# Kernel tuning notes

Hardware: AMD Instinct MI355X
Metric: run time of the kernel (lower is better)

## Reference

```python
import jax, jax.numpy as jnp
import numpy as np

N_NODES = 50000
N_EDGES = 800000
IN_CH = 128
HID_CH = 128
OUT_CH = 10
NUM_GRAPHS = 128


def setup_inputs() -> dict:
    key = jax.random.key(0)
    ks = jax.random.split(key, 10)
    x = jax.random.normal(ks[0], (N_NODES, IN_CH), dtype=jnp.float32)
    edge_index = jax.random.randint(ks[1], (2, N_EDGES), 0, N_NODES, dtype=jnp.int64)
    batch = jnp.sort(jax.random.randint(ks[2], (N_NODES,), 0, NUM_GRAPHS, dtype=jnp.int64))
    s1 = 1.0 / np.sqrt(IN_CH)
    s2 = 1.0 / np.sqrt(HID_CH)
    W1 = jax.random.uniform(ks[3], (IN_CH, HID_CH), jnp.float32, -s1, s1)
    b1 = jnp.zeros((HID_CH,), jnp.float32)
    W2 = jax.random.uniform(ks[4], (HID_CH, HID_CH), jnp.float32, -s2, s2)
    b2 = jnp.zeros((HID_CH,), jnp.float32)
    Wc = jax.random.uniform(ks[5], (HID_CH, OUT_CH), jnp.float32, -s2, s2)
    bc = jax.random.uniform(ks[6], (OUT_CH,), jnp.float32, -s2, s2)
    return {"x": x, "edge_index": edge_index, "batch": batch,
            "W1": W1, "b1": b1, "W2": W2, "b2": b2, "Wc": Wc, "bc": bc}


def _gcn_norm(edge_index, num_nodes):
    # add self-loops, compute symmetric normalization deg^-1/2[src]*deg^-1/2[dst]
    loop = jnp.arange(num_nodes, dtype=edge_index.dtype)
    src = jnp.concatenate([edge_index[0], loop])
    dst = jnp.concatenate([edge_index[1], loop])
    deg = jax.ops.segment_sum(jnp.ones_like(dst, dtype=jnp.float32), dst,
                              num_segments=num_nodes)
    dinv = jnp.where(deg > 0, jax.lax.rsqrt(deg), 0.0)
    norm = dinv[src] * dinv[dst]
    return src, dst, norm


def _gcn_conv(h, src, dst, norm, W, b, num_nodes):
    h = h @ W                                    # [N, out]
    msg = h[src] * norm[:, None]                 # [E+N, out] gather + scale
    agg = jax.ops.segment_sum(msg, dst, num_segments=num_nodes)
    return agg + b


def reference(x, edge_index, batch, W1, b1, W2, b2, Wc, bc):
    n = x.shape[0]
    src, dst, norm = _gcn_norm(edge_index, n)
    h = jax.nn.relu(_gcn_conv(x, src, dst, norm, W1, b1, n))
    h = jax.nn.relu(_gcn_conv(h, src, dst, norm, W2, b2, n))
    # global mean pool over graphs
    sums = jax.ops.segment_sum(h, batch, num_segments=NUM_GRAPHS)
    cnts = jax.ops.segment_sum(jnp.ones((n,), jnp.float32), batch,
                               num_segments=NUM_GRAPHS)
    pooled = sums / jnp.maximum(cnts, 1.0)[:, None]
    # dropout is identity in eval mode
    return pooled @ Wc + bc
```

## Files before the change

### kernel.cpp

```cpp
#include <hip/hip_runtime.h>

#define N_NODES 50000
#define N_EDGES 800000
#define CH 128
#define NOUT 10
#define NUM_GRAPHS 128
#define GR 64
#define GEMM_BLOCKS ((N_NODES + GR - 1) / GR)
#define FILL_SEGS 200
#define FILL_CHUNK (N_EDGES / FILL_SEGS)
#define FILL_BLOCKS (FILL_SEGS * 8)
#define DST_RANGE (N_NODES / 8)
#define DEG_CAP 64

typedef __attribute__((ext_vector_type(8))) short bf16x8;
typedef __attribute__((ext_vector_type(4))) float f32x4;

union FragU { uint4 u; bf16x8 s; };

__device__ __forceinline__ unsigned pack_bf16(float a, float b) {
    unsigned ua = __float_as_uint(a), ub = __float_as_uint(b);
    ua += 0x7fffu + ((ua >> 16) & 1u);
    ub += 0x7fffu + ((ub >> 16) & 1u);
    return (ua >> 16) | (ub & 0xffff0000u);
}

__device__ __forceinline__ unsigned short cvt_bf16(float v) {
    unsigned u = __float_as_uint(v);
    u += 0x7fffu + ((u >> 16) & 1u);
    return (unsigned short)(u >> 16);
}

__global__ __launch_bounds__(256) void k_prep(const float* __restrict__ W1,
                                              const float* __restrict__ W2,
                                              unsigned short* __restrict__ Wb1,
                                              unsigned short* __restrict__ Wb2,
                                              int* __restrict__ fill_pos,
                                              float* __restrict__ psum) {
    if (blockIdx.x < 2) {
        const float* W = blockIdx.x ? W2 : W1;
        unsigned short* Wb = blockIdx.x ? Wb2 : Wb1;
        for (int i = threadIdx.x; i < CH * CH; i += 256) {
            int k = i >> 7, n = i & 127;
            Wb[((((k >> 3) << 7) + n) << 3) + (k & 7)] = cvt_bf16(W[i]);
        }
    } else if (blockIdx.x < 198) {
        int idx = (blockIdx.x - 2) * 256 + threadIdx.x;
        if (idx < N_NODES) fill_pos[idx] = 0;
    } else {
        psum[(blockIdx.x - 198) * 256 + threadIdx.x] = 0.f;
    }
}

template <bool SCALE, bool ABF16>
__device__ __forceinline__ void gemm_body9(const void* __restrict__ X,
                                           const unsigned short* __restrict__ Wb,
                                           unsigned short* __restrict__ Yb,
                                           const int* __restrict__ cnt,
                                           int bid) {
    const int tid = threadIdx.x;
    const int w = tid >> 6;
    const int lane = tid & 63;
    const int m = lane & 15;
    const int quad = lane >> 4;
    const int row0 = bid * GR + w * 16;

    int row_a = row0 + m;
    if (row_a > N_NODES - 1) row_a = N_NODES - 1;

    FragU af[4];
    if (ABF16) {
        const uint4* Xr = (const uint4*)((const unsigned short*)X + (size_t)row_a * CH);
        #pragma unroll
        for (int ks = 0; ks < 4; ++ks) af[ks].u = Xr[ks * 4 + quad];
    } else {
        const float4* Xr = (const float4*)((const float*)X + (size_t)row_a * CH) + quad * 2;
        float4 a[8];
        #pragma unroll
        for (int ks = 0; ks < 4; ++ks) {
            a[ks * 2]     = Xr[ks * 8];
            a[ks * 2 + 1] = Xr[ks * 8 + 1];
        }
        #pragma unroll
        for (int ks = 0; ks < 4; ++ks) {
            af[ks].u.x = pack_bf16(a[ks * 2].x, a[ks * 2].y);
            af[ks].u.y = pack_bf16(a[ks * 2].z, a[ks * 2].w);
            af[ks].u.z = pack_bf16(a[ks * 2 + 1].x, a[ks * 2 + 1].y);
            af[ks].u.w = pack_bf16(a[ks * 2 + 1].z, a[ks * 2 + 1].w);
        }
    }

    f32x4 acc[8];
    #pragma unroll
    for (int ct = 0; ct < 8; ++ct) acc[ct] = (f32x4){0.f, 0.f, 0.f, 0.f};

    const uint4* Wq = (const uint4*)Wb;
    #pragma unroll
    for (int ks = 0; ks < 4; ++ks) {
        const int kg = ks * 4 + quad;
        #pragma unroll
        for (int ct = 0; ct < 8; ++ct) {
            FragU bfu;
            bfu.u = Wq[kg * 128 + m * 8 + ct];
            acc[ct] = __builtin_amdgcn_mfma_f32_16x16x32_bf16(af[ks].s, bfu.s, acc[ct], 0, 0, 0);
        }
    }

    #pragma unroll
    for (int r = 0; r < 4; ++r) {
        int row = row0 + quad * 4 + r;
        if (row < N_NODES) {
            float s = SCALE ? rsqrtf((float)(cnt[row] + 1)) : 1.0f;
            uint4 o;
            o.x = pack_bf16(acc[0][r] * s, acc[1][r] * s);
            o.y = pack_bf16(acc[2][r] * s, acc[3][r] * s);
            o.z = pack_bf16(acc[4][r] * s, acc[5][r] * s);
            o.w = pack_bf16(acc[6][r] * s, acc[7][r] * s);
            *(uint4*)(Yb + (size_t)row * CH + m * 8) = o;
        }
    }
}

__global__ __launch_bounds__(256) void k_gemm_fill(const float* __restrict__ X,
                                                   const unsigned short* __restrict__ Wb,
                                                   unsigned short* __restrict__ Yb,
                                                   const int* __restrict__ src,
                                                   const int* __restrict__ dst,
                                                   int* __restrict__ fill_pos,
                                                   int* __restrict__ csr_src) {
    if (blockIdx.x < FILL_BLOCKS) {
        const int b = blockIdx.x;
        const int rng = b & 7;
        const int seg = b >> 3;
        const int lo = rng * DST_RANGE, hi = lo + DST_RANGE;
        const int base = seg * FILL_CHUNK;
        for (int it = threadIdx.x * 4; it < FILL_CHUNK; it += 1024) {
            int e = base + it;
            int4 d4 = *(const int4*)(dst + e);
            int4 s4 = *(const int4*)(src + e);
            #pragma unroll
            for (int k = 0; k < 4; ++k) {
                int d = (&d4.x)[k];
                if (d >= lo && d < hi) {
                    int slot = atomicAdd(&fill_pos[d], 1);
                    if (slot < DEG_CAP) csr_src[(d << 6) + slot] = (&s4.x)[k];
                }
            }
        }
    } else {
        gemm_body9<false, false>(X, Wb, Yb, nullptr, blockIdx.x - FILL_BLOCKS);
    }
}

__global__ __launch_bounds__(256) void k_gemm9b(const unsigned short* __restrict__ Xb,
                                                const unsigned short* __restrict__ Wb,
                                                unsigned short* __restrict__ Yb,
                                                const int* __restrict__ cnt) {
    gemm_body9<true, true>(Xb, Wb, Yb, cnt, blockIdx.x);
}

__device__ __forceinline__ void acc_row(float (&x)[8], uint4 q, float w) {
    #pragma unroll
    for (int t = 0; t < 4; ++t) {
        unsigned r = ((const unsigned*)&q)[t];
        x[2 * t]     = fmaf(w, __uint_as_float(r << 16), x[2 * t]);
        x[2 * t + 1] = fmaf(w, __uint_as_float(r & 0xffff0000u), x[2 * t + 1]);
    }
}

template <bool HAS_W, bool POOL>
__device__ __forceinline__ void gather_body(const unsigned* __restrict__ tb,
                                            const int* __restrict__ csr_src,
                                            const int* __restrict__ cnt,
                                            const float* __restrict__ bias,
                                            unsigned short* __restrict__ hb,
                                            const int* __restrict__ batch,
                                            float* __restrict__ psum) {
    const int wid = threadIdx.x >> 6;
    const int lane = threadIdx.x & 63;
    const int sub = lane >> 4;
    const int cidx = lane & 15;
    const int v = blockIdx.x * 4 + wid;

    int lenc = cnt[v];
    const float dv = rsqrtf((float)(lenc + 1));
    int len = lenc > DEG_CAP ? DEG_CAP : lenc;

    int u_l = 0;
    float w_l = 0.f;
    if (lane < len) {
        u_l = csr_src[(v << 6) + lane];
        if (HAS_W) w_l = rsqrtf((float)(cnt[u_l] + 1));
    }

    const uint4* tbq = (const uint4*)tb;
    float x[8];
    #pragma unroll
    for (int t = 0; t < 8; ++t) x[t] = 0.f;

    const int ng = (len + 3) >> 2;
    for (int g = 0; g < ng; g += 4) {
        uint4 q0, q1, q2, q3;
        float w0, w1, w2, w3;
        bool h1 = g + 1 < ng, h2 = g + 2 < ng, h3 = g + 3 < ng;
        {
            int idx = g * 4 + sub; bool act = idx < len; int ic = act ? idx : 0;
            int u = __shfl(u_l, ic);
            w0 = act ? (HAS_W ? __shfl(w_l, ic) : 1.f) : 0.f;
            q0 = tbq[(size_t)u * 16 + cidx];
        }
        if (h1) {
            int idx = (g + 1) * 4 + sub; bool act = idx < len; int ic = act ? idx : 0;
            int u = __shfl(u_l, ic);
            w1 = act ? (HAS_W ? __shfl(w_l, ic) : 1.f) : 0.f;
            q1 = tbq[(size_t)u * 16 + cidx];
        }
        if (h2) {
            int idx = (g + 2) * 4 + sub; bool act = idx < len; int ic = act ? idx : 0;
            int u = __shfl(u_l, ic);
            w2 = act ? (HAS_W ? __shfl(w_l, ic) : 1.f) : 0.f;
            q2 = tbq[(size_t)u * 16 + cidx];
        }
        if (h3) {
            int idx = (g + 3) * 4 + sub; bool act = idx < len; int ic = act ? idx : 0;
            int u = __shfl(u_l, ic);
            w3 = act ? (HAS_W ? __shfl(w_l, ic) : 1.f) : 0.f;
            q3 = tbq[(size_t)u * 16 + cidx];
        }
        acc_row(x, q0, w0);
        if (h1) acc_row(x, q1, w1);
        if (h2) acc_row(x, q2, w2);
        if (h3) acc_row(x, q3, w3);
    }
    {
        uint4 q = tbq[(size_t)v * 16 + cidx];
        float w = (sub == 0) ? (HAS_W ? dv : 1.f) : 0.f;
        acc_row(x, q, w);
    }

    #pragma unroll
    for (int t = 0; t < 8; ++t) {
        x[t] += __shfl_xor(x[t], 16);
        x[t] += __shfl_xor(x[t], 32);
    }

    const float4* b4 = (const float4*)bias;
    float4 b0 = b4[cidx * 2], b1 = b4[cidx * 2 + 1];
    float o[8];
    o[0] = fmaxf(fmaf(dv, x[0], b0.x), 0.f);
    o[1] = fmaxf(fmaf(dv, x[1], b0.y), 0.f);
    o[2] = fmaxf(fmaf(dv, x[2], b0.z), 0.f);
    o[3] = fmaxf(fmaf(dv, x[3], b0.w), 0.f);
    o[4] = fmaxf(fmaf(dv, x[4], b1.x), 0.f);
    o[5] = fmaxf(fmaf(dv, x[5], b1.y), 0.f);
    o[6] = fmaxf(fmaf(dv, x[6], b1.z), 0.f);
    o[7] = fmaxf(fmaf(dv, x[7], b1.w), 0.f);

    if (POOL) {
        __shared__ float sh[4][128];
        __shared__ int sg[4];
        if (lane == 0) sg[wid] = batch[v];
        if (sub == 0) {
            float4* shp = (float4*)&sh[wid][cidx * 8];
            shp[0] = (float4){o[0], o[1], o[2], o[3]};
            shp[1] = (float4){o[4], o[5], o[6], o[7]};
        }
        __syncthreads();
        const int tid = threadIdx.x;
        if (tid < 128) {
            int g0 = sg[0], g1 = sg[1], g2 = sg[2], g3 = sg[3];
            float v0 = sh[0][tid], v1 = sh[1][tid], v2 = sh[2][tid], v3 = sh[3][tid];
            if (g0 == g3) {
                atomicAdd(&psum[g0 * CH + tid], v0 + v1 + v2 + v3);
            } else {
                if (g0 == g1) v1 += v0; else atomicAdd(&psum[g0 * CH + tid], v0);
                if (g1 == g2) v2 += v1; else atomicAdd(&psum[g1 * CH + tid], v1);
                if (g2 == g3) v3 += v2; else atomicAdd(&psum[g2 * CH + tid], v2);
                atomicAdd(&psum[g3 * CH + tid], v3);
            }
        }
    } else {
        if (sub == 0) {
            uint4 ob;
            ob.x = pack_bf16(o[0], o[1]);
            ob.y = pack_bf16(o[2], o[3]);
            ob.z = pack_bf16(o[4], o[5]);
            ob.w = pack_bf16(o[6], o[7]);
            *(uint4*)(hb + (size_t)v * CH + cidx * 8) = ob;
        }
    }
}

__global__ __launch_bounds__(256) void k_gather_hw(const unsigned* __restrict__ tb,
                                                   const int* __restrict__ csr_src,
                                                   const int* __restrict__ cnt,
                                                   const float* __restrict__ b,
                                                   unsigned short* __restrict__ hb) {
    gather_body<true, false>(tb, csr_src, cnt, b, hb, nullptr, nullptr);
}

__global__ __launch_bounds__(256) void k_gather_pool(const unsigned* __restrict__ tb,
                                                     const int* __restrict__ csr_src,
                                                     const int* __restrict__ cnt,
                                                     const float* __restrict__ b,
                                                     const int* __restrict__ batch,
                                                     float* __restrict__ psum) {
    gather_body<false, true>(tb, csr_src, cnt, b, nullptr, batch, psum);
}

__global__ __launch_bounds__(128) void k_classify(const float* __restrict__ psum,
                                                  const int* __restrict__ batch,
                                                  const float* __restrict__ Wc,
                                                  const float* __restrict__ bc,
                                                  float* __restrict__ out) {
    __shared__ float p[CH];
    __shared__ float sinv;
    int g = blockIdx.x;
    int tid = threadIdx.x;
    if (tid == 0) {
        int lo = 0, hi = N_NODES;
        while (lo < hi) { int mid = (lo + hi) >> 1; if (batch[mid] < g) lo = mid + 1; else hi = mid; }
        int start = lo;
        lo = 0; hi = N_NODES;
        while (lo < hi) { int mid = (lo + hi) >> 1; if (batch[mid] < g + 1) lo = mid + 1; else hi = mid; }
        sinv = 1.0f / fmaxf((float)(lo - start), 1.0f);
    }
    __syncthreads();
    p[tid] = psum[g * CH + tid] * sinv;
    __syncthreads();
    if (tid < NOUT) {
        float acc = bc[tid];
        #pragma unroll 4
        for (int k = 0; k < CH; ++k) acc += p[k] * Wc[k * NOUT + tid];
        out[g * NOUT + tid] = acc;
    }
}

extern "C" void kernel_launch(void* const* d_in, const int* in_sizes, int n_in,
                              void* d_out, int out_size, void* d_ws, size_t ws_size,
                              hipStream_t stream) {
    const float* x     = (const float*)d_in[0];
    const int*   ei    = (const int*)d_in[1];
    const int*   batch = (const int*)d_in[2];
    const float* W1    = (const float*)d_in[3];
    const float* b1    = (const float*)d_in[4];
    const float* W2    = (const float*)d_in[5];
    const float* b2    = (const float*)d_in[6];
    const float* Wc    = (const float*)d_in[7];
    const float* bc    = (const float*)d_in[8];
    float* out = (float*)d_out;

    const int* src = ei;
    const int* dst = ei + N_EDGES;

    int*            fill_pos = (int*)d_ws;
    int*            csr_src  = fill_pos + N_NODES;
    unsigned short* wb1      = (unsigned short*)(csr_src + (size_t)N_NODES * DEG_CAP);
    unsigned short* wb2      = wb1 + CH * CH;
    unsigned short* tb       = wb2 + CH * CH;
    unsigned short* hb16     = tb + (size_t)N_NODES * CH;
    float*          psum     = (float*)(hb16 + (size_t)N_NODES * CH);

    k_prep<<<198 + 64, 256, 0, stream>>>(W1, W2, wb1, wb2, fill_pos, psum);

    k_gemm_fill<<<FILL_BLOCKS + GEMM_BLOCKS, 256, 0, stream>>>(
        x, wb1, tb, src, dst, fill_pos, csr_src);

    k_gather_hw<<<N_NODES / 4, 256, 0, stream>>>((unsigned*)tb, csr_src, fill_pos, b1, hb16);

    k_gemm9b<<<GEMM_BLOCKS, 256, 0, stream>>>(hb16, wb2, tb, fill_pos);

    k_gather_pool<<<N_NODES / 4, 256, 0, stream>>>((unsigned*)tb, csr_src, fill_pos, b2,
                                                   batch, psum);

    k_classify<<<NUM_GRAPHS, 128, 0, stream>>>(psum, batch, Wc, bc, out);
}
```

Before: 260.7 us.

## Reorder gemm/fill blocks, batch fill loads, widen gather prefetch depth

The fused gemm+CSR-fill kernel now puts the GEMM blocks first. Fill blocks are regrouped into 4 destination ranges instead of 8, so each edge chunk is scanned fewer times. The fill loop issues all its int4 loads before doing the atomics, which gives more memory-level parallelism. The gather kernels unroll the neighbor loads 8 deep instead of 4, raising outstanding loads at the cost of more registers and possible occupancy loss.

```diff
diff --git a/kernel.cpp b/kernel.cpp
--- a/kernel.cpp
+++ b/kernel.cpp
@@ -7,10 +7,11 @@
 #define NUM_GRAPHS 128
 #define GR 64
 #define GEMM_BLOCKS ((N_NODES + GR - 1) / GR)
+#define RANGES 4
 #define FILL_SEGS 200
 #define FILL_CHUNK (N_EDGES / FILL_SEGS)
-#define FILL_BLOCKS (FILL_SEGS * 8)
-#define DST_RANGE (N_NODES / 8)
+#define FILL_BLOCKS (FILL_SEGS * RANGES)
+#define DST_RANGE (N_NODES / RANGES)
 #define DEG_CAP 64
 
 typedef __attribute__((ext_vector_type(8))) short bf16x8;
@@ -128,27 +129,39 @@
                                                    const int* __restrict__ dst,
                                                    int* __restrict__ fill_pos,
                                                    int* __restrict__ csr_src) {
-    if (blockIdx.x < FILL_BLOCKS) {
-        const int b = blockIdx.x;
-        const int rng = b & 7;
-        const int seg = b >> 3;
+    if (blockIdx.x < GEMM_BLOCKS) {
+        gemm_body9<false, false>(X, Wb, Yb, nullptr, blockIdx.x);
+    } else {
+        const int b = blockIdx.x - GEMM_BLOCKS;
+        const int t = (b + (GEMM_BLOCKS & 7)) & 7;
+        const int rng = t >> 1;
+        const int seg = ((b >> 3) << 1) | (t & 1);
         const int lo = rng * DST_RANGE, hi = lo + DST_RANGE;
         const int base = seg * FILL_CHUNK;
-        for (int it = threadIdx.x * 4; it < FILL_CHUNK; it += 1024) {
-            int e = base + it;
-            int4 d4 = *(const int4*)(dst + e);
-            int4 s4 = *(const int4*)(src + e);
-            #pragma unroll
-            for (int k = 0; k < 4; ++k) {
-                int d = (&d4.x)[k];
-                if (d >= lo && d < hi) {
-                    int slot = atomicAdd(&fill_pos[d], 1);
-                    if (slot < DEG_CAP) csr_src[(d << 6) + slot] = (&s4.x)[k];
+
+        int4 d4[4], s4[4];
+        #pragma unroll
+        for (int i = 0; i < 4; ++i) {
+            int off = (i * 256 + threadIdx.x) * 4;
+            if (off < FILL_CHUNK) {
+                d4[i] = *(const int4*)(dst + base + off);
+                s4[i] = *(const int4*)(src + base + off);
+            }
+        }
+        #pragma unroll
+        for (int i = 0; i < 4; ++i) {
+            int off = (i * 256 + threadIdx.x) * 4;
+            if (off < FILL_CHUNK) {
+                #pragma unroll
+                for (int k = 0; k < 4; ++k) {
+                    int d = (&d4[i].x)[k];
+                    if (d >= lo && d < hi) {
+                        int slot = atomicAdd(&fill_pos[d], 1);
+                        if (slot < DEG_CAP) csr_src[(d << 6) + slot] = (&s4[i].x)[k];
+                    }
                 }
             }
         }
-    } else {
-        gemm_body9<false, false>(X, Wb, Yb, nullptr, blockIdx.x - FILL_BLOCKS);
     }
 }
 
@@ -199,38 +212,23 @@
     for (int t = 0; t < 8; ++t) x[t] = 0.f;
 
     const int ng = (len + 3) >> 2;
-    for (int g = 0; g < ng; g += 4) {
-        uint4 q0, q1, q2, q3;
-        float w0, w1, w2, w3;
-        bool h1 = g + 1 < ng, h2 = g + 2 < ng, h3 = g + 3 < ng;
-        {
-            int idx = g * 4 + sub; bool act = idx < len; int ic = act ? idx : 0;
-            int u = __shfl(u_l, ic);
-            w0 = act ? (HAS_W ? __shfl(w_l, ic) : 1.f) : 0.f;
-            q0 = tbq[(size_t)u * 16 + cidx];
-        }
-        if (h1) {
-            int idx = (g + 1) * 4 + sub; bool act = idx < len; int ic = act ? idx : 0;
-            int u = __shfl(u_l, ic);
-            w1 = act ? (HAS_W ? __shfl(w_l, ic) : 1.f) : 0.f;
-            q1 = tbq[(size_t)u * 16 + cidx];
-        }
-        if (h2) {
-            int idx = (g + 2) * 4 + sub; bool act = idx < len; int ic = act ? idx : 0;
-            int u = __shfl(u_l, ic);
-            w2 = act ? (HAS_W ? __shfl(w_l, ic) : 1.f) : 0.f;
-            q2 = tbq[(size_t)u * 16 + cidx];
-        }
-        if (h3) {
-            int idx = (g + 3) * 4 + sub; bool act = idx < len; int ic = act ? idx : 0;
-            int u = __shfl(u_l, ic);
-            w3 = act ? (HAS_W ? __shfl(w_l, ic) : 1.f) : 0.f;
-            q3 = tbq[(size_t)u * 16 + cidx];
-        }
-        acc_row(x, q0, w0);
-        if (h1) acc_row(x, q1, w1);
-        if (h2) acc_row(x, q2, w2);
-        if (h3) acc_row(x, q3, w3);
+    for (int g = 0; g < ng; g += 8) {
+        uint4 q[8];
+        float w[8];
+        #pragma unroll
+        for (int k = 0; k < 8; ++k) {
+            if (g + k < ng) {
+                int idx = (g + k) * 4 + sub;
+                bool act = idx < len;
+                int ic = act ? idx : 0;
+                int u = __shfl(u_l, ic);
+                w[k] = act ? (HAS_W ? __shfl(w_l, ic) : 1.f) : 0.f;
+                q[k] = tbq[(size_t)u * 16 + cidx];
+            }
+        }
+        #pragma unroll
+        for (int k = 0; k < 8; ++k)
+            if (g + k < ng) acc_row(x, q[k], w[k]);
     }
     {
         uint4 q = tbq[(size_t)v * 16 + cidx];
@@ -363,7 +361,7 @@
 
     k_prep<<<198 + 64, 256, 0, stream>>>(W1, W2, wb1, wb2, fill_pos, psum);
 
-    k_gemm_fill<<<FILL_BLOCKS + GEMM_BLOCKS, 256, 0, stream>>>(
+    k_gemm_fill<<<GEMM_BLOCKS + FILL_BLOCKS, 256, 0, stream>>>(
         x, wb1, tb, src, dst, fill_pos, csr_src);
 
     k_gather_hw<<<N_NODES / 4, 256, 0, stream>>>((unsigned*)tb, csr_src, fill_pos, b1, hb16);
```

After: 261.2 us. No clear change (+0.2%).
